# Kernel tuning notes

Hardware: AMD Instinct MI355X
Metric: run time of the kernel (lower is better)

Reference implementation:

```python
import jax, jax.numpy as jnp
import numpy as np

B, P, T = 64, 49, 20      # batch, num_pixels (7x7), caption length
V, E, D, A, ENC = 32000, 512, 512, 512, 2048


def setup_inputs() -> dict:
    key = jax.random.key(0)
    ks = jax.random.split(key, 20)
    s = 0.02
    return {
        "features": jax.random.normal(ks[0], (B, P, ENC), jnp.float32),
        "captions": jax.random.randint(ks[1], (B, T), 0, V, jnp.int64),
        "embed_table": jax.random.normal(ks[2], (V, E), jnp.float32) * s,
        "W_ih": jax.random.normal(ks[3], (4 * D, ENC + E), jnp.float32) * s,
        "b_ih": jnp.zeros((4 * D,), jnp.float32),
        "W_hh": jax.random.normal(ks[4], (4 * D, D), jnp.float32) * s,
        "b_hh": jnp.zeros((4 * D,), jnp.float32),
        "W_init_h": jax.random.normal(ks[5], (ENC, D), jnp.float32) * s,
        "b_init_h": jnp.zeros((D,), jnp.float32),
        "W_init_c": jax.random.normal(ks[6], (ENC, D), jnp.float32) * s,
        "b_init_c": jnp.zeros((D,), jnp.float32),
        "W_enc_att": jax.random.normal(ks[7], (ENC, A), jnp.float32) * s,
        "b_enc_att": jnp.zeros((A,), jnp.float32),
        "W_dec_att": jax.random.normal(ks[8], (D, A), jnp.float32) * s,
        "b_dec_att": jnp.zeros((A,), jnp.float32),
        "w_A": jax.random.normal(ks[9], (A,), jnp.float32) * s,
        "b_A": jnp.zeros((), jnp.float32),
        "W_out": jax.random.normal(ks[10], (D, V), jnp.float32) * s,
        "b_out": jnp.zeros((V,), jnp.float32),
    }


def reference(features, captions, embed_table, W_ih, b_ih, W_hh, b_hh,
              W_init_h, b_init_h, W_init_c, b_init_c,
              W_enc_att, b_enc_att, W_dec_att, b_dec_att, w_A, b_A,
              W_out, b_out):
    # Dropout is treated as identity (eval mode) for a deterministic baseline.
    bsz, seq_len = captions.shape
    emb = embed_table[captions]                              # [B,T,E]
    mean_f = features.mean(axis=1)                           # [B,ENC]
    h0 = mean_f @ W_init_h + b_init_h                        # [B,D]
    c0 = mean_f @ W_init_c + b_init_c                        # [B,D]
    enc_states = features @ W_enc_att + b_enc_att            # [B,P,A] (precomputed, loop-invariant)

    def step(carry, x_t):
        h, c = carry
        dec = h @ W_dec_att + b_dec_att                      # [B,A]
        comb = jnp.tanh(enc_states + dec[:, None, :])        # [B,P,A]
        scores = comb @ w_A + b_A                            # [B,P]
        alpha = jax.nn.softmax(scores, axis=1)
        ctx = jnp.einsum('bpe,bp->be', features, alpha)      # [B,ENC]
        x = jnp.concatenate([ctx, x_t], axis=1)              # [B,ENC+E]
        gates = x @ W_ih.T + b_ih + h @ W_hh.T + b_hh        # [B,4D]
        i, f, g, o = jnp.split(gates, 4, axis=1)
        i, f, o = jax.nn.sigmoid(i), jax.nn.sigmoid(f), jax.nn.sigmoid(o)
        g = jnp.tanh(g)
        c2 = f * c + i * g
        h2 = o * jnp.tanh(c2)
        logits = h2 @ W_out + b_out                          # [B,V]
        return (h2, c2), logits

    xs = jnp.swapaxes(emb[:, :seq_len - 1], 0, 1)            # [T-1,B,E]
    _, preds = jax.lax.scan(step, (h0, c0), xs)              # [T-1,B,V]
    preds = jnp.swapaxes(preds, 0, 1)                        # [B,T-1,V]
    vocab = W_out.shape[1]
    last = jnp.zeros((bsz, 1, vocab), preds.dtype)           # t = T-1 never written
    return jnp.concatenate([preds, last], axis=1)            # [B,T,V]
```

## Files before the change

### kernel.cpp

```cpp
#include <hip/hip_runtime.h>

constexpr int B_   = 64;
constexpr int P_   = 49;
constexpr int T_   = 20;
constexpr int V_   = 32000;
constexpr int E_   = 512;
constexpr int D_   = 512;
constexpr int A_   = 512;
constexpr int ENC_ = 2048;
constexpr int NT_  = T_ - 1;
constexpr int KX_  = ENC_ + E_ + D_;
constexpr int KSPL = 8;
constexpr int GCH  = (KX_ / 64) / KSPL;

#define DI __device__ __forceinline__

using u16 = unsigned short;
typedef short   bf16x8 __attribute__((ext_vector_type(8)));
typedef float   f32x4  __attribute__((ext_vector_type(4)));
typedef u16     u16x4  __attribute__((ext_vector_type(4)));
typedef u16     u16x2  __attribute__((ext_vector_type(2)));

DI float sigm(float x) { return 1.0f / (1.0f + __expf(-x)); }
DI float tanhx(float x) {
  x = fminf(15.0f, fmaxf(-15.0f, x));
  float e = __expf(2.0f * x);
  return (e - 1.0f) / (e + 1.0f);
}
DI u16 f2bf(float x) {
  union { float f; unsigned u; } v{x};
  unsigned r = v.u + 0x7FFF + ((v.u >> 16) & 1);
  return (u16)(r >> 16);
}
DI float bf2f(u16 x) {
  union { unsigned u; float f; } v;
  v.u = ((unsigned)x) << 16;
  return v.f;
}
DI f32x4 mfma16(bf16x8 a, bf16x8 b, f32x4 c) {
  return __builtin_amdgcn_mfma_f32_16x16x32_bf16(a, b, c, 0, 0, 0);
}


__global__ __launch_bounds__(256) void k_mean_bf(const float* __restrict__ feat,
                                                 u16* __restrict__ mfb) {
  int idx = blockIdx.x * 256 + threadIdx.x;
  int b = idx >> 11, e = idx & (ENC_ - 1);
  const float* f = feat + (size_t)b * P_ * ENC_ + e;
  float s = 0.f;
#pragma unroll
  for (int p = 0; p < P_; p++) s += f[(size_t)p * ENC_];
  mfb[idx] = f2bf(s * (1.0f / P_));
}

__global__ __launch_bounds__(256) void k_tr_cvt(const float* __restrict__ in,
    u16* __restrict__ outp, int R, int C) {
  __shared__ float tbuf[32][33];
  int tx = threadIdx.x & 31, ty = threadIdx.x >> 5;
  int c0 = blockIdx.x * 32, r0 = blockIdx.y * 32;
#pragma unroll
  for (int i = 0; i < 4; i++)
    tbuf[ty + 8 * i][tx] = in[(size_t)(r0 + ty + 8 * i) * C + c0 + tx];
  __syncthreads();
#pragma unroll
  for (int i = 0; i < 4; i++)
    outp[(size_t)(c0 + ty + 8 * i) * R + r0 + tx] = f2bf(tbuf[tx][ty + 8 * i]);
}

__global__ __launch_bounds__(256) void k_cvt4(const float* __restrict__ in,
                                              u16* __restrict__ o) {
  int i = blockIdx.x * 256 + threadIdx.x;
  float4 v = ((const float4*)in)[i];
  u16x4 r = {f2bf(v.x), f2bf(v.y), f2bf(v.z), f2bf(v.w)};
  ((u16x4*)o)[i] = r;
}

__global__ __launch_bounds__(256) void k_wg4(const float* __restrict__ Wih,
    const float* __restrict__ Whh, u16* __restrict__ Wg) {
  int i = blockIdx.x * 256 + threadIdx.x;
  int j = i / 768, rem = i - j * 768;
  int k = rem * 4;
  const float* src = (k < ENC_ + E_) ? (Wih + (size_t)j * (ENC_ + E_) + k)
                                     : (Whh + (size_t)j * D_ + (k - ENC_ - E_));
  float4 v = *(const float4*)src;
  u16x4 r = {f2bf(v.x), f2bf(v.y), f2bf(v.z), f2bf(v.w)};
  ((u16x4*)Wg)[i] = r;
}

__global__ __launch_bounds__(256) void k_emb_bf(const int* __restrict__ cap,
    const float* __restrict__ tab, u16* __restrict__ embb) {
  int idx = blockIdx.x * 256 + threadIdx.x;
  int e = idx & (E_ - 1);
  int tb = idx >> 9;
  int b = tb & 63, t = tb >> 6;
  embb[idx] = f2bf(tab[(size_t)cap[b * T_ + t] * E_ + e]);
}

__global__ __launch_bounds__(256) void k_init_bf(const u16* __restrict__ mfb,
    const u16* __restrict__ WiT, const float* __restrict__ binh,
    const float* __restrict__ binc, u16* __restrict__ hbf, float* __restrict__ c) {
  int wid = threadIdx.x >> 6, lane = threadIdx.x & 63;
  int n0 = blockIdx.x * 64 + wid * 16;
  int l16 = lane & 15, lk = lane >> 4;
  const u16* bp = WiT + (size_t)(n0 + l16) * ENC_ + 8 * lk;
  const u16* ap = mfb + (size_t)l16 * ENC_ + 8 * lk;
  f32x4 acc[4] = {};
#pragma unroll 4
  for (int kc = 0; kc < ENC_; kc += 32) {
    bf16x8 b = *(const bf16x8*)(bp + kc);
#pragma unroll
    for (int mf = 0; mf < 4; mf++) {
      bf16x8 a = *(const bf16x8*)(ap + (size_t)mf * 16 * ENC_ + kc);
      acc[mf] = mfma16(a, b, acc[mf]);
    }
  }
  int n = n0 + l16;
#pragma unroll
  for (int mf = 0; mf < 4; mf++) {
    int m = mf * 16 + 4 * lk;
#pragma unroll
    for (int r = 0; r < 4; r++) {
      float v = acc[mf][r];
      if (n < D_) hbf[(size_t)(m + r) * D_ + n] = f2bf(v + binh[n]);
      else        c[(size_t)(m + r) * D_ + (n - D_)] = v + binc[n - D_];
    }
  }
}


__global__ __launch_bounds__(256) void k_enc_bf(const u16* __restrict__ fb,
    const u16* __restrict__ WeT, const float* __restrict__ benc,
    float* __restrict__ encs) {
  int wid = threadIdx.x >> 6, lane = threadIdx.x & 63;
  int m0 = blockIdx.x * 64, n0 = blockIdx.y * 64 + wid * 16;
  int l16 = lane & 15, lk = lane >> 4;
  const u16* ap = fb + (size_t)(m0 + l16) * ENC_ + 8 * lk;
  const u16* bp = WeT + (size_t)(n0 + l16) * ENC_ + 8 * lk;
  f32x4 acc[4] = {};
#pragma unroll 8
  for (int i = 0; i < ENC_ / 32; i++) {
    int kc = i * 32;
    bf16x8 b = *(const bf16x8*)(bp + kc);
#pragma unroll
    for (int mf = 0; mf < 4; mf++) {
      bf16x8 a = *(const bf16x8*)(ap + (size_t)mf * 16 * ENC_ + kc);
      acc[mf] = mfma16(a, b, acc[mf]);
    }
  }
  float bv = benc[n0 + l16];
#pragma unroll
  for (int mf = 0; mf < 4; mf++) {
    int m = m0 + mf * 16 + 4 * lk;
#pragma unroll
    for (int r = 0; r < 4; r++)
      encs[(size_t)(m + r) * A_ + n0 + l16] = acc[mf][r] + bv;
  }
}

__global__ __launch_bounds__(256) void k_gates_bf(const u16* __restrict__ ctxb,
    const u16* __restrict__ embb, const u16* __restrict__ hbf,
    const u16* __restrict__ Wg, float* __restrict__ gp, int t) {
  int wid = threadIdx.x >> 6, lane = threadIdx.x & 63;
  int j0 = blockIdx.x * 64 + wid * 16;
  int sp = blockIdx.y;
  int l16 = lane & 15, lk = lane >> 4;
  const u16* bp = Wg + (size_t)(j0 + l16) * KX_ + 8 * lk;
  f32x4 acc[4] = {};
#pragma unroll
  for (int i = 0; i < KX_ / KSPL / 32; i++) {
    int kc = sp * (KX_ / KSPL) + i * 32;
    int k = kc + 8 * lk;
    bf16x8 b = *(const bf16x8*)(bp + kc);
#pragma unroll
    for (int mf = 0; mf < 4; mf++) {
      int row = mf * 16 + l16;
      const u16* src;
      if (k < ENC_)            src = ctxb + (size_t)row * ENC_ + k;
      else if (k < ENC_ + E_)  src = embb + ((size_t)t * B_ + row) * E_ + (k - ENC_);
      else                     src = hbf + (size_t)row * D_ + (k - ENC_ - E_);
      bf16x8 a = *(const bf16x8*)src;
      acc[mf] = mfma16(a, b, acc[mf]);
    }
  }
#pragma unroll
  for (int mf = 0; mf < 4; mf++) {
    int m = mf * 16 + 4 * lk;
#pragma unroll
    for (int r = 0; r < 4; r++)
      gp[((size_t)sp * B_ + m + r) * (4 * D_) + j0 + l16] = acc[mf][r];
  }
}

__global__ __launch_bounds__(256) void k_logits_all3(const u16* __restrict__ hall,
    const u16* __restrict__ WoT, const float* __restrict__ bout,
    float* __restrict__ out) {
  __shared__ float tile[64 * 68];
  int bid = blockIdx.x;
  int x8 = bid & 7, g = bid >> 3;
  int sg = g & 3, ntg = g >> 2;
  int nt = x8 + 8 * ntg;
  if (nt >= 500) return;
  int wid = threadIdx.x >> 6, lane = threadIdx.x & 63;
  int n0 = nt * 64 + wid * 16;
  int l16 = lane & 15, lk = lane >> 4;
  const u16* bp = WoT + (size_t)(n0 + l16) * D_ + 8 * lk;
  float bv = bout[n0 + l16];
  int tr = threadIdx.x >> 2, tc = threadIdx.x & 3;
#pragma unroll 1
  for (int s = sg; s < NT_; s += 4) {
    const u16* ap = hall + (size_t)s * B_ * D_ + (size_t)l16 * D_ + 8 * lk;
    f32x4 acc[4] = {};
#pragma unroll
    for (int kc = 0; kc < 16; kc++) {
      bf16x8 b = *(const bf16x8*)(bp + kc * 32);
#pragma unroll
      for (int mf = 0; mf < 4; mf++) {
        bf16x8 a = *(const bf16x8*)(ap + (size_t)mf * 16 * D_ + kc * 32);
        acc[mf] = mfma16(a, b, acc[mf]);
      }
    }
    __syncthreads();
#pragma unroll
    for (int mf = 0; mf < 4; mf++)
#pragma unroll
      for (int r = 0; r < 4; r++)
        tile[(mf * 16 + 4 * lk + r) * 68 + wid * 16 + l16] = acc[mf][r] + bv;
    __syncthreads();
    float* op = out + ((size_t)tr * T_ + s) * V_ + nt * 64;
#pragma unroll
    for (int j = 0; j < 4; j++) {
      int cc = (tc + j * 4) * 4;
      *(float4*)(op + cc) = *(float4*)&tile[tr * 68 + cc];
    }
  }
  if (sg == 3) {
    float4 z = {0.f, 0.f, 0.f, 0.f};
    float* op = out + ((size_t)tr * T_ + (T_ - 1)) * V_ + nt * 64;
#pragma unroll
    for (int j = 0; j < 4; j++) *(float4*)(op + (tc + j * 4) * 4) = z;
  }
}


__global__ __launch_bounds__(512) void k_att3(const u16* __restrict__ featb,
    const float* __restrict__ encs, const u16* __restrict__ WdT,
    const float* __restrict__ bdec, const float* __restrict__ wA,
    const float* __restrict__ bA, const float* __restrict__ gp,
    const float* __restrict__ bih, const float* __restrict__ bhh,
    const float* __restrict__ c_in, float* __restrict__ c_out,
    u16* __restrict__ hbf, u16* __restrict__ hallp, u16* __restrict__ ctxb,
    int do_reduce, int do_att) {
  __shared__ u16 hsb[D_];
  __shared__ float ds[A_];
  __shared__ float sc[P_];
  __shared__ float inv_s;
  int b = blockIdx.x, y = blockIdx.y, tid = threadIdx.x;

  if (do_reduce) {
    int d = tid;
    float g0 = 0, g1 = 0, g2 = 0, g3 = 0;
#pragma unroll
    for (int s = 0; s < KSPL; s++) {
      const float* g = gp + (size_t)(s * B_ + b) * (4 * D_);
      g0 += g[d]; g1 += g[D_ + d]; g2 += g[2 * D_ + d]; g3 += g[3 * D_ + d];
    }
    g0 += bih[d] + bhh[d];
    g1 += bih[D_ + d] + bhh[D_ + d];
    g2 += bih[2 * D_ + d] + bhh[2 * D_ + d];
    g3 += bih[3 * D_ + d] + bhh[3 * D_ + d];
    float iv = sigm(g0), fv = sigm(g1), gv = tanhx(g2), ov = sigm(g3);
    float cv = fmaf(fv, c_in[b * D_ + d], iv * gv);
    float hv = ov * tanhx(cv);
    u16 hb = f2bf(hv);
    hsb[d] = hb;
    if (y == 0) {
      c_out[b * D_ + d] = cv;
      hbf[b * D_ + d] = hb;
      hallp[b * D_ + d] = hb;
    }
  } else {
    hsb[tid] = hbf[b * D_ + tid];
  }
  __syncthreads();
  if (!do_att) return;

  {
    int w = tid >> 6, lane = tid & 63, l16 = lane & 15, lk = lane >> 4;
#pragma unroll
    for (int f = 0; f < 4; f++) {
      int n = w * 64 + f * 16 + l16;
      const u16* bp = WdT + (size_t)n * D_ + 8 * lk;
      f32x4 acc = {};
#pragma unroll
      for (int kc = 0; kc < D_; kc += 32) {
        bf16x8 av = *(const bf16x8*)(hsb + kc + 8 * lk);
        bf16x8 bv = *(const bf16x8*)(bp + kc);
        acc = mfma16(av, bv, acc);
      }
      if (lk == 0) ds[n] = acc[0] + bdec[n];
    }
  }
  __syncthreads();

  int wv_ = tid >> 6, ln = tid & 63;
  float bA0 = bA[0];
  for (int p = wv_; p < P_; p += 8) {
    const float* ep = encs + (size_t)(b * P_ + p) * A_;
    float s = 0.f;
#pragma unroll
    for (int a = ln; a < A_; a += 64) s += tanhx(ep[a] + ds[a]) * wA[a];
#pragma unroll
    for (int off = 32; off; off >>= 1) s += __shfl_down(s, off);
    if (ln == 0) sc[p] = s + bA0;
  }
  __syncthreads();

  if (tid == 0) {
    float mx = -1e30f;
    for (int p = 0; p < P_; p++) mx = fmaxf(mx, sc[p]);
    float sum = 0.f;
    for (int p = 0; p < P_; p++) { float ex = __expf(sc[p] - mx); sc[p] = ex; sum += ex; }
    inv_s = 1.0f / sum;
  }
  __syncthreads();

  {
    float inv = inv_s;
    int e = y * 1024 + tid * 2;
    const u16* fp = featb + (size_t)b * P_ * ENC_ + e;
    float s0 = 0.f, s1 = 0.f;
#pragma unroll
    for (int p = 0; p < P_; p++) {
      u16x2 w = *(const u16x2*)(fp + (size_t)p * ENC_);
      s0 = fmaf(bf2f(w.x), sc[p], s0);
      s1 = fmaf(bf2f(w.y), sc[p], s1);
    }
    u16x2 o = {f2bf(s0 * inv), f2bf(s1 * inv)};
    *(u16x2*)(ctxb + b * ENC_ + e) = o;
  }
}


DI int swz(int row, int slot) { return row * 64 + ((slot ^ (row >> 2)) << 2); }

__global__ __launch_bounds__(256) void k_mean(const float* __restrict__ feat,
                                              float* __restrict__ mf) {
  int idx = blockIdx.x * 256 + threadIdx.x;
  int b = idx >> 11, e = idx & (ENC_ - 1);
  const float* f = feat + (size_t)b * P_ * ENC_ + e;
  float s = 0.f;
#pragma unroll
  for (int p = 0; p < P_; p++) s += f[(size_t)p * ENC_];
  mf[idx] = s * (1.0f / P_);
}

__global__ __launch_bounds__(256) void k_emb(const int* __restrict__ cap,
                                             const float* __restrict__ tab,
                                             float* __restrict__ emb) {
  int idx = blockIdx.x * 256 + threadIdx.x;
  int e  = idx & (E_ - 1);
  int bt = idx >> 9;
  int b = bt / NT_, t = bt - b * NT_;
  int tok = cap[b * T_ + t];
  emb[idx] = tab[(size_t)tok * E_ + e];
}

__global__ __launch_bounds__(256) void k_init(const float* __restrict__ mf,
    const float* __restrict__ Wh, const float* __restrict__ bh,
    const float* __restrict__ Wc, const float* __restrict__ bc,
    float* __restrict__ h, float* __restrict__ c) {
  __shared__ float ms[ENC_];
  int b = blockIdx.y;
  for (int i = threadIdx.x; i < ENC_; i += 256) ms[i] = mf[b * ENC_ + i];
  __syncthreads();
  int d = blockIdx.x * 256 + threadIdx.x;
  const float* W = blockIdx.z ? Wc : Wh;
  float s = (blockIdx.z ? bc : bh)[d];
#pragma unroll 8
  for (int e = 0; e < ENC_; e++) s = fmaf(ms[e], W[(size_t)e * D_ + d], s);
  (blockIdx.z ? c : h)[b * D_ + d] = s;
}

__global__ __launch_bounds__(256) void k_zero_last(float* __restrict__ out) {
  int i = blockIdx.x * 256 + threadIdx.x;
  int b = i / 8000, v4 = i - b * 8000;
  float4 z = {0.f, 0.f, 0.f, 0.f};
  *(float4*)(out + ((size_t)b * T_ + (T_ - 1)) * V_ + (size_t)v4 * 4) = z;
}

__global__ __launch_bounds__(256) void k_enc(const float* __restrict__ Ag,
    const float* __restrict__ Wg, const float* __restrict__ bias,
    float* __restrict__ Cg) {
  __shared__ float As[64 * 64], Ws[64 * 64];
  int m0 = blockIdx.x * 64, n0 = blockIdx.y * 64;
  int tid = threadIdx.x, tn = tid & 15, tm = tid >> 4;
  float acc[4][4] = {};
#pragma unroll 1
  for (int ch = 0; ch < ENC_ / 64; ch++) {
    int k0 = ch * 64;
    __syncthreads();
#pragma unroll
    for (int q = 0; q < 4; q++) {
      int idx = tid + q * 256;
      int row = idx >> 4, slot = idx & 15;
      *(float4*)&As[swz(row, slot)] =
          *(const float4*)(Ag + (size_t)(m0 + row) * ENC_ + k0 + slot * 4);
      *(float4*)&Ws[swz(row, slot)] =
          *(const float4*)(Wg + (size_t)(k0 + row) * A_ + n0 + slot * 4);
    }
    __syncthreads();
#pragma unroll
    for (int kk = 0; kk < 16; kk++) {
      float4 av[4], wv[4];
#pragma unroll
      for (int i = 0; i < 4; i++) av[i] = *(float4*)&As[swz(4 * tm + i, kk)];
#pragma unroll
      for (int u = 0; u < 4; u++) wv[u] = *(float4*)&Ws[swz(4 * kk + u, tn)];
      const float* wq = (const float*)wv;
#pragma unroll
      for (int i = 0; i < 4; i++) {
        const float* aq = (const float*)&av[i];
#pragma unroll
        for (int j = 0; j < 4; j++) {
          float s = acc[i][j];
#pragma unroll
          for (int u = 0; u < 4; u++) s = fmaf(aq[u], wq[u * 4 + j], s);
          acc[i][j] = s;
        }
      }
    }
  }
#pragma unroll
  for (int i = 0; i < 4; i++) {
    int m = m0 + 4 * tm + i, n = n0 + 4 * tn;
    float4 bv = *(const float4*)(bias + n);
    float4 o = {acc[i][0] + bv.x, acc[i][1] + bv.y, acc[i][2] + bv.z, acc[i][3] + bv.w};
    *(float4*)(Cg + (size_t)m * A_ + n) = o;
  }
}

__global__ __launch_bounds__(256) void k_logits(const float* __restrict__ h,
    const float* __restrict__ Wout, const float* __restrict__ bout,
    float* __restrict__ out, int t) {
  __shared__ float As[64 * 64], Ws[64 * 64];
  int n0 = blockIdx.x * 64;
  int tid = threadIdx.x, tn = tid & 15, tm = tid >> 4;
  float acc[4][4] = {};
#pragma unroll 1
  for (int ch = 0; ch < D_ / 64; ch++) {
    int k0 = ch * 64;
    __syncthreads();
#pragma unroll
    for (int q = 0; q < 4; q++) {
      int idx = tid + q * 256;
      int row = idx >> 4, slot = idx & 15;
      *(float4*)&As[swz(row, slot)] =
          *(const float4*)(h + (size_t)row * D_ + k0 + slot * 4);
      *(float4*)&Ws[swz(row, slot)] =
          *(const float4*)(Wout + (size_t)(k0 + row) * V_ + n0 + slot * 4);
    }
    __syncthreads();
#pragma unroll
    for (int kk = 0; kk < 16; kk++) {
      float4 av[4], wv[4];
#pragma unroll
      for (int i = 0; i < 4; i++) av[i] = *(float4*)&As[swz(4 * tm + i, kk)];
#pragma unroll
      for (int u = 0; u < 4; u++) wv[u] = *(float4*)&Ws[swz(4 * kk + u, tn)];
      const float* wq = (const float*)wv;
#pragma unroll
      for (int i = 0; i < 4; i++) {
        const float* aq = (const float*)&av[i];
#pragma unroll
        for (int j = 0; j < 4; j++) {
          float s = acc[i][j];
#pragma unroll
          for (int u = 0; u < 4; u++) s = fmaf(aq[u], wq[u * 4 + j], s);
          acc[i][j] = s;
        }
      }
    }
  }
#pragma unroll
  for (int i = 0; i < 4; i++) {
    int m = 4 * tm + i, n = n0 + 4 * tn;
    float4 bv = *(const float4*)(bout + n);
    float4 o = {acc[i][0] + bv.x, acc[i][1] + bv.y, acc[i][2] + bv.z, acc[i][3] + bv.w};
    *(float4*)(out + ((size_t)m * T_ + t) * V_ + n) = o;
  }
}

__global__ __launch_bounds__(256) void k_gates(const float* __restrict__ ctx,
    const float* __restrict__ emb, const float* __restrict__ h,
    const float* __restrict__ Wih, const float* __restrict__ Whh,
    float* __restrict__ gp, int t) {
  __shared__ float As[64 * 64], Ws[64 * 64];
  int n0 = blockIdx.x * 64;
  int sp = blockIdx.y;
  int tid = threadIdx.x, tn = tid & 15, tm = tid >> 4;
  float acc[4][4] = {};
#pragma unroll 1
  for (int ch = 0; ch < GCH; ch++) {
    int k0 = sp * (GCH * 64) + ch * 64;
    __syncthreads();
#pragma unroll
    for (int q = 0; q < 4; q++) {
      int idx = tid + q * 256;
      int row = idx >> 4, slot = idx & 15;
      int k = k0 + slot * 4;
      float4 xv;
      if (k < ENC_)            xv = *(const float4*)(ctx + (size_t)row * ENC_ + k);
      else if (k < ENC_ + E_)  xv = *(const float4*)(emb + ((size_t)row * NT_ + t) * E_ + (k - ENC_));
      else                     xv = *(const float4*)(h + (size_t)row * D_ + (k - ENC_ - E_));
      *(float4*)&As[swz(row, slot)] = xv;
      int j = n0 + row;
      float4 wv2;
      if (k < ENC_ + E_) wv2 = *(const float4*)(Wih + (size_t)j * (ENC_ + E_) + k);
      else               wv2 = *(const float4*)(Whh + (size_t)j * D_ + (k - ENC_ - E_));
      *(float4*)&Ws[swz(row, slot)] = wv2;
    }
    __syncthreads();
#pragma unroll
    for (int kk = 0; kk < 16; kk++) {
      float4 av[4], wv[4];
#pragma unroll
      for (int i = 0; i < 4; i++) av[i] = *(float4*)&As[swz(4 * tm + i, kk)];
#pragma unroll
      for (int j = 0; j < 4; j++) wv[j] = *(float4*)&Ws[swz(4 * tn + j, kk)];
#pragma unroll
      for (int i = 0; i < 4; i++) {
        const float* aq = (const float*)&av[i];
#pragma unroll
        for (int j = 0; j < 4; j++) {
          const float* wqj = (const float*)&wv[j];
          float s = acc[i][j];
#pragma unroll
          for (int u = 0; u < 4; u++) s = fmaf(aq[u], wqj[u], s);
          acc[i][j] = s;
        }
      }
    }
  }
#pragma unroll
  for (int i = 0; i < 4; i++) {
    int b = 4 * tm + i, j = n0 + 4 * tn;
    float4 o = {acc[i][0], acc[i][1], acc[i][2], acc[i][3]};
    *(float4*)(gp + ((size_t)(sp * B_ + b)) * (4 * D_) + j) = o;
  }
}

__global__ __launch_bounds__(512) void k_att(const float* __restrict__ feat,
    const float* __restrict__ encs, const float* __restrict__ Wdec,
    const float* __restrict__ bdec, const float* __restrict__ wA,
    const float* __restrict__ bA, const float* __restrict__ gp,
    const float* __restrict__ bih, const float* __restrict__ bhh,
    float* __restrict__ h, float* __restrict__ c, float* __restrict__ ctx,
    int do_reduce, int do_att) {
  __shared__ float hs[D_];
  __shared__ float ds[A_];
  __shared__ float sc[P_];
  __shared__ float inv_s;
  int b = blockIdx.x, tid = threadIdx.x;

  if (do_reduce) {
    int d = tid;
    float g0 = 0, g1 = 0, g2 = 0, g3 = 0;
#pragma unroll
    for (int s = 0; s < KSPL; s++) {
      const float* g = gp + (size_t)(s * B_ + b) * (4 * D_);
      g0 += g[d]; g1 += g[D_ + d]; g2 += g[2 * D_ + d]; g3 += g[3 * D_ + d];
    }
    g0 += bih[d] + bhh[d];
    g1 += bih[D_ + d] + bhh[D_ + d];
    g2 += bih[2 * D_ + d] + bhh[2 * D_ + d];
    g3 += bih[3 * D_ + d] + bhh[3 * D_ + d];
    float iv = sigm(g0), fv = sigm(g1), gv = tanhx(g2), ov = sigm(g3);
    float cv = fmaf(fv, c[b * D_ + d], iv * gv);
    float hv = ov * tanhx(cv);
    c[b * D_ + d] = cv;
    h[b * D_ + d] = hv;
    hs[d] = hv;
  } else {
    hs[tid] = h[b * D_ + tid];
  }
  __syncthreads();
  if (!do_att) return;

  {
    int a = tid;
    float s = bdec[a];
#pragma unroll 8
    for (int d = 0; d < D_; d++) s = fmaf(hs[d], Wdec[(size_t)d * A_ + a], s);
    ds[a] = s;
  }
  __syncthreads();

  int wv_ = tid >> 6, ln = tid & 63;
  float bA0 = bA[0];
  for (int p = wv_; p < P_; p += 8) {
    const float* ep = encs + (size_t)(b * P_ + p) * A_;
    float s = 0.f;
#pragma unroll
    for (int a = ln; a < A_; a += 64) s += tanhx(ep[a] + ds[a]) * wA[a];
#pragma unroll
    for (int off = 32; off; off >>= 1) s += __shfl_down(s, off);
    if (ln == 0) sc[p] = s + bA0;
  }
  __syncthreads();

  if (tid == 0) {
    float mx = -1e30f;
    for (int p = 0; p < P_; p++) mx = fmaxf(mx, sc[p]);
    float sum = 0.f;
    for (int p = 0; p < P_; p++) { float ex = __expf(sc[p] - mx); sc[p] = ex; sum += ex; }
    inv_s = 1.0f / sum;
  }
  __syncthreads();

  float inv = inv_s;
  for (int e = tid; e < ENC_; e += 512) {
    const float* fp = feat + (size_t)b * P_ * ENC_ + e;
    float s = 0.f;
#pragma unroll
    for (int p = 0; p < P_; p++) s = fmaf(fp[(size_t)p * ENC_], sc[p], s);
    ctx[b * ENC_ + e] = s * inv;
  }
}


extern "C" void kernel_launch(void* const* d_in, const int* in_sizes, int n_in,
                              void* d_out, int out_size, void* d_ws, size_t ws_size,
                              hipStream_t stream) {
  const float* features = (const float*)d_in[0];
  const int*   captions = (const int*)d_in[1];
  const float* table    = (const float*)d_in[2];
  const float* Wih  = (const float*)d_in[3];
  const float* bih  = (const float*)d_in[4];
  const float* Whh  = (const float*)d_in[5];
  const float* bhh  = (const float*)d_in[6];
  const float* Winh = (const float*)d_in[7];
  const float* binh = (const float*)d_in[8];
  const float* Winc = (const float*)d_in[9];
  const float* binc = (const float*)d_in[10];
  const float* Wenc = (const float*)d_in[11];
  const float* benc = (const float*)d_in[12];
  const float* Wdec = (const float*)d_in[13];
  const float* bdec = (const float*)d_in[14];
  const float* wA   = (const float*)d_in[15];
  const float* bA   = (const float*)d_in[16];
  const float* Wout = (const float*)d_in[17];
  const float* bout = (const float*)d_in[18];
  float* out = (float*)d_out;

  constexpr size_t F_ENC = (size_t)B_ * P_ * A_;
  constexpr size_t F_C   = (size_t)B_ * D_;
  constexpr size_t F_GP  = (size_t)KSPL * B_ * 4 * D_;
  constexpr size_t U_WOT = (size_t)V_ * D_;
  constexpr size_t U_WG  = (size_t)(4 * D_) * KX_;
  constexpr size_t U_HBF = (size_t)B_ * D_;
  constexpr size_t U_CTX = (size_t)B_ * ENC_;
  constexpr size_t U_FEAT = (size_t)B_ * P_ * ENC_;
  constexpr size_t U_WET = (size_t)A_ * ENC_;
  constexpr size_t U_EMB = (size_t)NT_ * B_ * E_;
  constexpr size_t U_WDT = (size_t)A_ * D_;
  constexpr size_t U_HALL = (size_t)NT_ * B_ * D_;
  static_assert(U_EMB + U_WDT <= U_WET, "embb+WdT overlay WeT region");
  constexpr size_t NEED_BYTES =
      (F_ENC + 2 * F_C + F_GP) * 4 +
      (U_WOT + U_WG + U_HBF + U_CTX + U_FEAT + U_WET + U_HALL) * 2;

  if (ws_size >= NEED_BYTES) {
    float* ws = (float*)d_ws;
    float* enc_states = ws;
    float* cbuf0  = enc_states + F_ENC;
    float* cbuf1  = cbuf0 + F_C;
    float* gparts = cbuf1 + F_C;
    u16* WoT   = (u16*)(gparts + F_GP);
    u16* Wg    = WoT + U_WOT;
    u16* hbf   = Wg + U_WG;
    u16* ctxb  = hbf + U_HBF;
    u16* featb = ctxb + U_CTX;
    u16* wetr  = featb + U_FEAT;
    u16* WeT   = wetr;
    u16* embb  = wetr;
    u16* WdT   = wetr + U_EMB;
    u16* hall  = wetr + U_WET;
    u16* WiT   = (u16*)gparts;
    u16* mfb   = ctxb;
    float* cb[2] = {cbuf0, cbuf1};

    k_mean_bf<<<512, 256, 0, stream>>>(features, mfb);
    k_tr_cvt<<<dim3(D_ / 32, ENC_ / 32), 256, 0, stream>>>(Winh, WiT, ENC_, D_);
    k_tr_cvt<<<dim3(D_ / 32, ENC_ / 32), 256, 0, stream>>>(Winc, WiT + (size_t)D_ * ENC_, ENC_, D_);
    k_init_bf<<<16, 256, 0, stream>>>(mfb, WiT, binh, binc, hbf, cbuf0);
    k_cvt4<<<(int)(U_FEAT / 4 / 256), 256, 0, stream>>>(features, featb);
    k_tr_cvt<<<dim3(A_ / 32, ENC_ / 32), 256, 0, stream>>>(Wenc, WeT, ENC_, A_);
    k_enc_bf<<<dim3(49, 8), 256, 0, stream>>>(featb, WeT, benc, enc_states);
    k_emb_bf<<<2432, 256, 0, stream>>>(captions, table, embb);
    k_tr_cvt<<<dim3(A_ / 32, D_ / 32), 256, 0, stream>>>(Wdec, WdT, D_, A_);
    k_tr_cvt<<<dim3(V_ / 32, D_ / 32), 256, 0, stream>>>(Wout, WoT, D_, V_);
    k_wg4<<<(int)(U_WG / 4 / 256), 256, 0, stream>>>(Wih, Whh, Wg);

    for (int t = 0; t < NT_; t++) {
      u16* hallp = (t > 0) ? (hall + (size_t)(t - 1) * B_ * D_) : hall;
      const float* cin = cb[(t > 0 ? (t - 1) : 0) & 1];
      float* cout = cb[t & 1];
      k_att3<<<dim3(64, 2), 512, 0, stream>>>(featb, enc_states, WdT, bdec, wA,
                                              bA, gparts, bih, bhh, cin, cout,
                                              hbf, hallp, ctxb, t > 0 ? 1 : 0, 1);
      k_gates_bf<<<dim3(32, KSPL), 256, 0, stream>>>(ctxb, embb, hbf, Wg, gparts, t);
    }
    k_att3<<<dim3(64, 1), 512, 0, stream>>>(featb, enc_states, WdT, bdec, wA,
                                            bA, gparts, bih, bhh,
                                            cb[(NT_ - 1) & 1], cb[NT_ & 1], hbf,
                                            hall + (size_t)(NT_ - 1) * B_ * D_,
                                            ctxb, 1, 0);
    k_logits_all3<<<2016, 256, 0, stream>>>(hall, WoT, bout, out);
  } else {
    float* ws = (float*)d_ws;
    float* enc_states = ws;
    float* mean_f = enc_states + (size_t)B_ * P_ * A_;
    float* emb    = mean_f + (size_t)B_ * ENC_;
    float* h      = emb + (size_t)B_ * NT_ * E_;
    float* c      = h + (size_t)B_ * D_;
    float* ctx    = c + (size_t)B_ * D_;
    float* gparts = ctx + (size_t)B_ * ENC_;

    k_mean<<<512, 256, 0, stream>>>(features, mean_f);
    k_emb<<<2432, 256, 0, stream>>>(captions, table, emb);
    k_init<<<dim3(2, 64, 2), 256, 0, stream>>>(mean_f, Winh, binh, Winc, binc, h, c);
    k_enc<<<dim3(49, 8), 256, 0, stream>>>(features, Wenc, benc, enc_states);
    k_zero_last<<<2000, 256, 0, stream>>>(out);

    for (int t = 0; t < NT_; t++) {
      k_att<<<64, 512, 0, stream>>>(features, enc_states, Wdec, bdec, wA, bA,
                                    gparts, bih, bhh, h, c, ctx, t > 0 ? 1 : 0, 1);
      if (t > 0)
        k_logits<<<500, 256, 0, stream>>>(h, Wout, bout, out, t - 1);
      k_gates<<<dim3(32, KSPL), 256, 0, stream>>>(ctx, emb, h, Wih, Whh, gparts, t);
    }
    k_att<<<64, 512, 0, stream>>>(features, enc_states, Wdec, bdec, wA, bA,
                                  gparts, bih, bhh, h, c, ctx, 1, 0);
    k_logits<<<500, 256, 0, stream>>>(h, Wout, bout, out, NT_ - 1);
  }
}
```

Baseline: 1.265 ms.

## Retile logits GEMM per timestep, add wide W_out transpose, hoist zeroing

The final logits kernel now gives each block one timestep and a 256-column vocabulary tile, with the B fragments held in registers and the whole tile staged in shared memory for wide coalesced stores. The W_out transpose and bf16 conversion move to a new kernel that uses 128x256 tiles and 16-byte stores instead of the generic 32x32 transpose. Zeroing of the last timestep moves to a separate kernel launched before the recurrence. The intent is better reuse of W_out loads and wider memory transactions, at the cost of a much larger shared-memory tile (about 67 KB) and higher register pressure, both of which may reduce occupancy.

```diff
diff --git a/kernel.cpp b/kernel.cpp
--- a/kernel.cpp
+++ b/kernel.cpp
@@ -67,6 +67,28 @@
     outp[(size_t)(c0 + ty + 8 * i) * R + r0 + tx] = f2bf(tbuf[tx][ty + 8 * i]);
 }
 
+__global__ __launch_bounds__(256) void k_trW(const float* __restrict__ in,
+                                             u16* __restrict__ outp) {
+  __shared__ u16 ld[128][264];
+  int v0 = blockIdx.x * 128, k0 = blockIdx.y * 256;
+  int vf = (threadIdx.x & 31) * 4, kk = threadIdx.x >> 5;
+#pragma unroll 4
+  for (int p = 0; p < 32; p++) {
+    int k = kk + p * 8;
+    float4 v = *(const float4*)(in + (size_t)(k0 + k) * V_ + v0 + vf);
+    ld[vf + 0][k] = f2bf(v.x);
+    ld[vf + 1][k] = f2bf(v.y);
+    ld[vf + 2][k] = f2bf(v.z);
+    ld[vf + 3][k] = f2bf(v.w);
+  }
+  __syncthreads();
+  int v = threadIdx.x >> 1, h = threadIdx.x & 1;
+  u16* op = outp + (size_t)(v0 + v) * D_ + k0 + h * 128;
+#pragma unroll
+  for (int i = 0; i < 16; i++)
+    *(bf16x8*)(op + i * 8) = *(const bf16x8*)(&ld[v][h * 128 + i * 8]);
+}
+
 __global__ __launch_bounds__(256) void k_cvt4(const float* __restrict__ in,
                                               u16* __restrict__ o) {
   int i = blockIdx.x * 256 + threadIdx.x;
@@ -94,6 +116,13 @@
   int tb = idx >> 9;
   int b = tb & 63, t = tb >> 6;
   embb[idx] = f2bf(tab[(size_t)cap[b * T_ + t] * E_ + e]);
+}
+
+__global__ __launch_bounds__(256) void k_zero_last(float* __restrict__ out) {
+  int i = blockIdx.x * 256 + threadIdx.x;
+  int b = i / 8000, v4 = i - b * 8000;
+  float4 z = {0.f, 0.f, 0.f, 0.f};
+  *(float4*)(out + ((size_t)b * T_ + (T_ - 1)) * V_ + (size_t)v4 * 4) = z;
 }
 
 __global__ __launch_bounds__(256) void k_init_bf(const u16* __restrict__ mfb,
@@ -191,53 +220,51 @@
   }
 }
 
-__global__ __launch_bounds__(256) void k_logits_all3(const u16* __restrict__ hall,
+__global__ __launch_bounds__(256) void k_logits_all4(const u16* __restrict__ hall,
     const u16* __restrict__ WoT, const float* __restrict__ bout,
     float* __restrict__ out) {
-  __shared__ float tile[64 * 68];
-  int bid = blockIdx.x;
-  int x8 = bid & 7, g = bid >> 3;
-  int sg = g & 3, ntg = g >> 2;
-  int nt = x8 + 8 * ntg;
-  if (nt >= 500) return;
-  int wid = threadIdx.x >> 6, lane = threadIdx.x & 63;
-  int n0 = nt * 64 + wid * 16;
+  __shared__ float tile[64 * 264];
+  int L = blockIdx.x;
+  int x8 = L & 7, r = L >> 3;
+  int g = r / 24, s = r % 24;
+  int nt = g * 8 + x8;
+  if (nt >= 125 || s >= NT_) return;
+  int w = threadIdx.x >> 6, lane = threadIdx.x & 63;
   int l16 = lane & 15, lk = lane >> 4;
-  const u16* bp = WoT + (size_t)(n0 + l16) * D_ + 8 * lk;
-  float bv = bout[n0 + l16];
+  const u16* ap0 = hall + (size_t)s * B_ * D_ + (size_t)l16 * D_ + 8 * lk;
+  int ncol0 = nt * 256 + w * 64;
+#pragma unroll 1
+  for (int ch = 0; ch < 4; ch++) {
+    int col = ncol0 + ch * 16 + l16;
+    const u16* bp = WoT + (size_t)col * D_ + 8 * lk;
+    bf16x8 bfr[16];
+#pragma unroll
+    for (int kc = 0; kc < 16; kc++) bfr[kc] = *(const bf16x8*)(bp + kc * 32);
+    f32x4 acc[4] = {};
+#pragma unroll
+    for (int kc = 0; kc < 16; kc++) {
+#pragma unroll
+      for (int mf = 0; mf < 4; mf++) {
+        bf16x8 a = *(const bf16x8*)(ap0 + (size_t)mf * 16 * D_ + kc * 32);
+        acc[mf] = mfma16(a, bfr[kc], acc[mf]);
+      }
+    }
+    float bv = bout[col];
+#pragma unroll
+    for (int mf = 0; mf < 4; mf++)
+#pragma unroll
+      for (int rr = 0; rr < 4; rr++)
+        tile[(mf * 16 + 4 * lk + rr) * 264 + w * 64 + ch * 16 + l16] =
+            acc[mf][rr] + bv;
+  }
+  __syncthreads();
   int tr = threadIdx.x >> 2, tc = threadIdx.x & 3;
-#pragma unroll 1
-  for (int s = sg; s < NT_; s += 4) {
-    const u16* ap = hall + (size_t)s * B_ * D_ + (size_t)l16 * D_ + 8 * lk;
-    f32x4 acc[4] = {};
-#pragma unroll
-    for (int kc = 0; kc < 16; kc++) {
-      bf16x8 b = *(const bf16x8*)(bp + kc * 32);
-#pragma unroll
-      for (int mf = 0; mf < 4; mf++) {
-        bf16x8 a = *(const bf16x8*)(ap + (size_t)mf * 16 * D_ + kc * 32);
-        acc[mf] = mfma16(a, b, acc[mf]);
-      }
-    }
-    __syncthreads();
-#pragma unroll
-    for (int mf = 0; mf < 4; mf++)
-#pragma unroll
-      for (int r = 0; r < 4; r++)
-        tile[(mf * 16 + 4 * lk + r) * 68 + wid * 16 + l16] = acc[mf][r] + bv;
-    __syncthreads();
-    float* op = out + ((size_t)tr * T_ + s) * V_ + nt * 64;
-#pragma unroll
-    for (int j = 0; j < 4; j++) {
-      int cc = (tc + j * 4) * 4;
-      *(float4*)(op + cc) = *(float4*)&tile[tr * 68 + cc];
-    }
-  }
-  if (sg == 3) {
-    float4 z = {0.f, 0.f, 0.f, 0.f};
-    float* op = out + ((size_t)tr * T_ + (T_ - 1)) * V_ + nt * 64;
-#pragma unroll
-    for (int j = 0; j < 4; j++) *(float4*)(op + (tc + j * 4) * 4) = z;
+  float* op = out + ((size_t)tr * T_ + s) * V_ + nt * 256;
+  const float* lp = &tile[tr * 264];
+#pragma unroll
+  for (int j = 0; j < 16; j++) {
+    int cc = (tc + j * 4) * 4;
+    *(float4*)(op + cc) = *(const float4*)(lp + cc);
   }
 }
 
@@ -379,13 +406,6 @@
 #pragma unroll 8
   for (int e = 0; e < ENC_; e++) s = fmaf(ms[e], W[(size_t)e * D_ + d], s);
   (blockIdx.z ? c : h)[b * D_ + d] = s;
-}
-
-__global__ __launch_bounds__(256) void k_zero_last(float* __restrict__ out) {
-  int i = blockIdx.x * 256 + threadIdx.x;
-  int b = i / 8000, v4 = i - b * 8000;
-  float4 z = {0.f, 0.f, 0.f, 0.f};
-  *(float4*)(out + ((size_t)b * T_ + (T_ - 1)) * V_ + (size_t)v4 * 4) = z;
 }
 
 __global__ __launch_bounds__(256) void k_enc(const float* __restrict__ Ag,
@@ -698,8 +718,9 @@
     k_enc_bf<<<dim3(49, 8), 256, 0, stream>>>(featb, WeT, benc, enc_states);
     k_emb_bf<<<2432, 256, 0, stream>>>(captions, table, embb);
     k_tr_cvt<<<dim3(A_ / 32, D_ / 32), 256, 0, stream>>>(Wdec, WdT, D_, A_);
-    k_tr_cvt<<<dim3(V_ / 32, D_ / 32), 256, 0, stream>>>(Wout, WoT, D_, V_);
+    k_trW<<<dim3(V_ / 128, D_ / 256), 256, 0, stream>>>(Wout, WoT);
     k_wg4<<<(int)(U_WG / 4 / 256), 256, 0, stream>>>(Wih, Whh, Wg);
+    k_zero_last<<<2000, 256, 0, stream>>>(out);
 
     for (int t = 0; t < NT_; t++) {
       u16* hallp = (t > 0) ? (hall + (size_t)(t - 1) * B_ * D_) : hall;
@@ -715,7 +736,7 @@
                                             cb[(NT_ - 1) & 1], cb[NT_ & 1], hbf,
                                             hall + (size_t)(NT_ - 1) * B_ * D_,
                                             ctxb, 1, 0);
-    k_logits_all3<<<2016, 256, 0, stream>>>(hall, WoT, bout, out);
+    k_logits_all4<<<3072, 256, 0, stream>>>(hall, WoT, bout, out);
   } else {
     float* ws = (float*)d_ws;
     float* enc_states = ws;
```

Result: faster. 1.208 ms (-4.5%).
